# Optimization experiments

Hardware: AMD Instinct MI355X
Metric: run time of the kernel (lower is better)

The kernel has to match this reference:

```python
import jax, jax.numpy as jnp
import numpy as np

N = [80000, 70000, 50000]   # entities per type (flattened over the ragged batch)
F = [64, 128, 48]           # feature width per entity type
D = 512                     # d_model
B = 64                      # number of episodes in the ragged batch
EPS_IN = 1e-4               # InputNorm eps
EPS_LN = 1e-5               # LayerNorm eps
CLIP = 5.0                  # InputNorm cliprange


def setup_inputs() -> dict:
    key = jax.random.key(0)
    ks = jax.random.split(key, 3 * 7 + 2)
    inp = {}
    for i, (n, f) in enumerate(zip(N, F)):
        base = 7 * i
        inp[f"ent{i}"] = jax.random.normal(ks[base], (n, f), dtype=jnp.float32)
        inp[f"mean{i}"] = 0.1 * jax.random.normal(ks[base + 1], (f,), dtype=jnp.float32)
        inp[f"var{i}"] = jax.random.uniform(ks[base + 2], (f,), minval=0.5, maxval=1.5, dtype=jnp.float32)
        inp[f"W{i}"] = jax.random.normal(ks[base + 3], (f, D), dtype=jnp.float32) / np.sqrt(f)
        inp[f"b{i}"] = jnp.zeros((D,), dtype=jnp.float32)
        inp[f"gamma{i}"] = jnp.ones((D,), dtype=jnp.float32)
        inp[f"beta{i}"] = jnp.zeros((D,), dtype=jnp.float32)
    total = sum(N)
    # index_map: permutation reassembling per-type blocks into ragged episode order
    inp["index_map"] = jax.random.permutation(ks[-2], total).astype(jnp.int64)
    inp["batch_index"] = jnp.sort(jax.random.randint(ks[-1], (total,), 0, B)).astype(jnp.int64)
    return inp


def _embed(x, mean, var, W, b, gamma, beta):
    # InputNorm: normalize with running stats, clip outliers
    h = jnp.clip((x - mean) * jax.lax.rsqrt(var + EPS_IN), -CLIP, CLIP)
    # Linear + ReLU
    h = jnp.maximum(h @ W + b, 0.0)
    # LayerNorm
    mu = h.mean(-1, keepdims=True)
    v = ((h - mu) ** 2).mean(-1, keepdims=True)
    return gamma * (h - mu) * jax.lax.rsqrt(v + EPS_LN) + beta


def reference(ent0, mean0, var0, W0, b0, gamma0, beta0,
              ent1, mean1, var1, W1, b1, gamma1, beta1,
              ent2, mean2, var2, W2, b2, gamma2, beta2,
              index_map, batch_index):
    embeds = [
        _embed(ent0, mean0, var0, W0, b0, gamma0, beta0),
        _embed(ent1, mean1, var1, W1, b1, gamma1, beta1),
        _embed(ent2, mean2, var2, W2, b2, gamma2, beta2),
    ]
    x = jnp.concatenate(embeds, axis=0)                      # [sum(N), D]
    entity_type = jnp.concatenate(
        [jnp.full((n, 1), float(i), dtype=jnp.float32) for i, n in enumerate(N)], axis=0
    )
    # ragged reorder: gather-based reassembly into episode-major order
    x = x[index_map]
    entity_types = entity_type[index_map]
    tbatch_index = batch_index[index_map]
    return x, tbatch_index, entity_types
```

## Files before the change

### kernel.cpp

```cpp
#include <hip/hip_runtime.h>

#define DMODEL 512
#define EPS_IN 1e-4f
#define EPS_LN 1e-5f
#define CLIPV  5.0f

typedef float f32x4 __attribute__((ext_vector_type(4)));
typedef short s16x8 __attribute__((ext_vector_type(8)));

__device__ __forceinline__ unsigned short f2bf(float f) {
    union { float f; unsigned u; } v; v.f = f;
    unsigned r = v.u + 0x7fffu + ((v.u >> 16) & 1u);
    return (unsigned short)(r >> 16);
}

struct TypeParams {
    const float* x;
    const float* ss;
    const unsigned short* Wt;
    const float* b; const float* gamma; const float* beta;
    int n;
    int offset;
    int nb;
};

__global__ __launch_bounds__(256) void setup_all(
    const int* __restrict__ index_map, const int* __restrict__ batch_index,
    int* __restrict__ inv, float* __restrict__ out_t, float* __restrict__ out_e,
    int total, int n0, int n01, int nbA,
    const float* __restrict__ W0, const float* __restrict__ W1, const float* __restrict__ W2,
    unsigned short* __restrict__ Wt0, unsigned short* __restrict__ Wt1, unsigned short* __restrict__ Wt2,
    const float* __restrict__ mean0, const float* __restrict__ var0,
    const float* __restrict__ mean1, const float* __restrict__ var1,
    const float* __restrict__ mean2, const float* __restrict__ var2,
    float* __restrict__ ss0, float* __restrict__ ss1, float* __restrict__ ss2)
{
    const int nbB = (DMODEL * 256) / 256;
    if (blockIdx.x < (unsigned)nbA) {
        const int j = blockIdx.x * 256 + threadIdx.x;
        if (j >= total) return;
        const int r = index_map[j];
        inv[r] = j;
        out_t[j] = (float)batch_index[r];
        out_e[j] = (r < n0) ? 0.0f : ((r < n01) ? 1.0f : 2.0f);
    } else if (blockIdx.x < (unsigned)(nbA + nbB)) {
        int idx = (blockIdx.x - nbA) * 256 + threadIdx.x;
        const float* W; unsigned short* Wt; int K, Kp;
        if (idx < DMODEL * 64)              { W = W0; Wt = Wt0; K = 64;  Kp = 64; }
        else if (idx < DMODEL * (64 + 128)) { idx -= DMODEL * 64;  W = W1; Wt = Wt1; K = 128; Kp = 128; }
        else                                { idx -= DMODEL * 192; W = W2; Wt = Wt2; K = 48;  Kp = 64; }
        const int nn = idx / Kp, k = idx - nn * Kp;
        const float w = (k < K) ? W[(size_t)k * DMODEL + nn] : 0.0f;
        Wt[idx] = f2bf(w);
    } else {
        const int c = threadIdx.x;
        if (c < 64)  { const float s = rsqrtf(var0[c] + EPS_IN); ss0[c] = s; ss0[64 + c]  = -mean0[c] * s; }
        if (c < 128) { const float s = rsqrtf(var1[c] + EPS_IN); ss1[c] = s; ss1[128 + c] = -mean1[c] * s; }
        if (c < 48)  { const float s = rsqrtf(var2[c] + EPS_IN); ss2[c] = s; ss2[48 + c]  = -mean2[c] * s; }
    }
}

template<int F, int KP>
__device__ __forceinline__ void embed_body(
    const TypeParams& p, int bid, const int* __restrict__ inv,
    float* __restrict__ out, char* lds)
{
    const int tid  = threadIdx.x;
    const int lane = tid & 63;
    const int wn   = tid >> 6;
    const int l15  = lane & 15;
    const int g    = lane >> 4;
    const int row0 = bid * 32;
    const int n    = p.n;
    constexpr int SEG = KP / 8;
    constexpr int NKS = KP / 32;

    float2* red = reinterpret_cast<float2*>(lds + NKS * 2048);

    if (tid < 32 * SEG) {
        const int r = tid & 31;
        const int s = tid >> 5;
        const int gr = row0 + r;
        const int c = s * 8;
        s16x8 pk;
#pragma unroll
        for (int jj = 0; jj < 8; ++jj) pk[jj] = 0;
        if (gr < n && c < F) {
            const float4 x0 = *(const float4*)(p.x + (size_t)gr * F + c);
            const float4 x1 = *(const float4*)(p.x + (size_t)gr * F + c + 4);
            const float4 sc0 = *(const float4*)(p.ss + c);
            const float4 sc1 = *(const float4*)(p.ss + c + 4);
            const float4 sh0 = *(const float4*)(p.ss + F + c);
            const float4 sh1 = *(const float4*)(p.ss + F + c + 4);
            float t[8];
            t[0] = fmaf(x0.x, sc0.x, sh0.x); t[1] = fmaf(x0.y, sc0.y, sh0.y);
            t[2] = fmaf(x0.z, sc0.z, sh0.z); t[3] = fmaf(x0.w, sc0.w, sh0.w);
            t[4] = fmaf(x1.x, sc1.x, sh1.x); t[5] = fmaf(x1.y, sc1.y, sh1.y);
            t[6] = fmaf(x1.z, sc1.z, sh1.z); t[7] = fmaf(x1.w, sc1.w, sh1.w);
#pragma unroll
            for (int jj = 0; jj < 8; ++jj)
                pk[jj] = (short)f2bf(fminf(fmaxf(t[jj], -CLIPV), CLIPV));
        }
        *reinterpret_cast<s16x8*>(lds + tid * 16) = pk;
    }
    __syncthreads();

    int orow[2];
#pragma unroll
    for (int m = 0; m < 2; ++m) {
        const int rg = row0 + m * 16 + l15;
        orow[m] = (rg < n) ? inv[p.offset + rg] : -1;
    }

    f32x4 acc[2][4];
#pragma unroll
    for (int m = 0; m < 2; ++m)
#pragma unroll
        for (int t = 0; t < 4; ++t) acc[m][t] = (f32x4)0.0f;

    const unsigned short* wtl = p.Wt + (size_t)(wn * 64 + l15) * KP + g * 8;

#pragma unroll
    for (int ks = 0; ks < NKS; ++ks) {
        const int ab = ((ks * 4 + g) * 32 + l15) * 16;
        const s16x8 a0 = *reinterpret_cast<const s16x8*>(lds + ab);
        const s16x8 a1 = *reinterpret_cast<const s16x8*>(lds + ab + 256);
#pragma unroll
        for (int t = 0; t < 4; ++t) {
            const s16x8 wf = *reinterpret_cast<const s16x8*>(wtl + (size_t)t * 16 * KP + ks * 32);
            acc[0][t] = __builtin_amdgcn_mfma_f32_16x16x32_bf16(wf, a0, acc[0][t], 0, 0, 0);
            acc[1][t] = __builtin_amdgcn_mfma_f32_16x16x32_bf16(wf, a1, acc[1][t], 0, 0, 0);
        }
    }

#pragma unroll
    for (int t = 0; t < 4; ++t) {
        const float4 bb = *(const float4*)(p.b + wn * 64 + t * 16 + g * 4);
#pragma unroll
        for (int m = 0; m < 2; ++m) {
            acc[m][t][0] = fmaxf(acc[m][t][0] + bb.x, 0.0f);
            acc[m][t][1] = fmaxf(acc[m][t][1] + bb.y, 0.0f);
            acc[m][t][2] = fmaxf(acc[m][t][2] + bb.z, 0.0f);
            acc[m][t][3] = fmaxf(acc[m][t][3] + bb.w, 0.0f);
        }
    }

    {
        float ps[2] = {0.0f, 0.0f}, pq[2] = {0.0f, 0.0f};
#pragma unroll
        for (int m = 0; m < 2; ++m)
#pragma unroll
            for (int t = 0; t < 4; ++t)
#pragma unroll
                for (int j = 0; j < 4; ++j) {
                    const float v = acc[m][t][j];
                    ps[m] += v;
                    pq[m] = fmaf(v, v, pq[m]);
                }
#pragma unroll
        for (int m = 0; m < 2; ++m) {
            ps[m] += __shfl_xor(ps[m], 16, 64);
            pq[m] += __shfl_xor(pq[m], 16, 64);
            ps[m] += __shfl_xor(ps[m], 32, 64);
            pq[m] += __shfl_xor(pq[m], 32, 64);
        }
        if (g == 0) {
#pragma unroll
            for (int m = 0; m < 2; ++m)
                red[(m * 16 + l15) * 8 + wn] = make_float2(ps[m], pq[m]);
        }
    }
    __syncthreads();

#pragma unroll
    for (int m = 0; m < 2; ++m) {
        const int od = orow[m];
        if (od < 0) continue;
        const int rl = m * 16 + l15;
        float s = 0.0f, q = 0.0f;
#pragma unroll
        for (int wq = 0; wq < 8; ++wq) { const float2 e = red[rl * 8 + wq]; s += e.x; q += e.y; }
        const float mu = s * (1.0f / DMODEL);
        const float vv = fmaxf(q * (1.0f / DMODEL) - mu * mu, 0.0f);
        const float sc = rsqrtf(vv + EPS_LN);
        float* op = out + (size_t)od * DMODEL + wn * 64 + g * 4;
#pragma unroll
        for (int t = 0; t < 4; ++t) {
            const float4 gg = *(const float4*)(p.gamma + wn * 64 + t * 16 + g * 4);
            const float4 ee = *(const float4*)(p.beta  + wn * 64 + t * 16 + g * 4);
            float4 o;
            o.x = fmaf(gg.x * sc, acc[m][t][0] - mu, ee.x);
            o.y = fmaf(gg.y * sc, acc[m][t][1] - mu, ee.y);
            o.z = fmaf(gg.z * sc, acc[m][t][2] - mu, ee.z);
            o.w = fmaf(gg.w * sc, acc[m][t][3] - mu, ee.w);
            *(float4*)(op + t * 16) = o;
        }
    }
}

__global__ __launch_bounds__(512, 6) void embed_all(
    TypeParams p0, TypeParams p1, TypeParams p2,
    const int* __restrict__ inv, float* __restrict__ out)
{
    extern __shared__ char lds[];
    const int bid = blockIdx.x;
    if (bid < p0.nb)                embed_body<64, 64>  (p0, bid, inv, out, lds);
    else if (bid < p0.nb + p1.nb)   embed_body<128, 128>(p1, bid - p0.nb, inv, out, lds);
    else                            embed_body<48, 64>  (p2, bid - p0.nb - p1.nb, inv, out, lds);
}

extern "C" void kernel_launch(void* const* d_in, const int* in_sizes, int n_in,
                              void* d_out, int out_size, void* d_ws, size_t ws_size,
                              hipStream_t stream)
{
    const int F0 = 64, F1 = 128, F2 = 48;
    const int n0 = in_sizes[0]  / F0;
    const int n1 = in_sizes[7]  / F1;
    const int n2 = in_sizes[14] / F2;
    const int total = n0 + n1 + n2;

    float* out   = (float*)d_out;
    float* out_t = out + (size_t)total * DMODEL;
    float* out_e = out_t + total;

    int* inv = (int*)d_ws;
    unsigned short* Wt0 = (unsigned short*)((char*)d_ws + (((size_t)total * 4 + 255) & ~(size_t)255));
    unsigned short* Wt1 = Wt0 + DMODEL * 64;
    unsigned short* Wt2 = Wt1 + DMODEL * 128;
    float* ss0 = (float*)(Wt2 + DMODEL * 64);
    float* ss1 = ss0 + 128;
    float* ss2 = ss1 + 256;

    const int* index_map   = (const int*)d_in[21];
    const int* batch_index = (const int*)d_in[22];

    const int nbA = (total + 255) / 256;
    const int nbB = (DMODEL * 256) / 256;
    setup_all<<<nbA + nbB + 1, 256, 0, stream>>>(
        index_map, batch_index, inv, out_t, out_e, total, n0, n0 + n1, nbA,
        (const float*)d_in[3], (const float*)d_in[10], (const float*)d_in[17],
        Wt0, Wt1, Wt2,
        (const float*)d_in[1],  (const float*)d_in[2],
        (const float*)d_in[8],  (const float*)d_in[9],
        (const float*)d_in[15], (const float*)d_in[16],
        ss0, ss1, ss2);

    TypeParams p0{(const float*)d_in[0],  ss0, Wt0,
                  (const float*)d_in[4],  (const float*)d_in[5],  (const float*)d_in[6],
                  n0, 0,       (n0 + 31) / 32};
    TypeParams p1{(const float*)d_in[7],  ss1, Wt1,
                  (const float*)d_in[11], (const float*)d_in[12], (const float*)d_in[13],
                  n1, n0,      (n1 + 31) / 32};
    TypeParams p2{(const float*)d_in[14], ss2, Wt2,
                  (const float*)d_in[18], (const float*)d_in[19], (const float*)d_in[20],
                  n2, n0 + n1, (n2 + 31) / 32};

    const int nb = p0.nb + p1.nb + p2.nb;
    const int lds_size = 4 * 2048 + 32 * 8 * sizeof(float2);
    embed_all<<<nb, 512, lds_size, stream>>>(p0, p1, p2, inv, out);
}
```

Before: 185.8 us.

## Build per-type compacted output-order lists so embed tiles write near-contiguous rows

Replaces the scattered inverse-permutation write with a per-block prefix-scan compaction. Each type gets a list of (output row, local input row) pairs, ordered by output position, and these are reserved with atomics. The embed kernel now walks tiles of this list, gathering input rows (small) and writing output rows in roughly increasing order instead of random order. This is meant to improve write locality for the large 512-wide output. It adds a zeroing kernel and atomic ordering that is not deterministic across blocks, and it lowers the occupancy hint from 6 to 4.

```diff
diff --git a/kernel.cpp b/kernel.cpp
--- a/kernel.cpp
+++ b/kernel.cpp
@@ -19,32 +19,85 @@
     const float* ss;
     const unsigned short* Wt;
     const float* b; const float* gamma; const float* beta;
-    int n;
-    int offset;
-    int nb;
+    const int2* jl;
 };
 
-__global__ __launch_bounds__(256) void setup_all(
+__global__ void zero_cur(int* cur) { if (threadIdx.x < 4) cur[threadIdx.x] = 0; }
+
+__global__ __launch_bounds__(256) void prep_all(
     const int* __restrict__ index_map, const int* __restrict__ batch_index,
-    int* __restrict__ inv, float* __restrict__ out_t, float* __restrict__ out_e,
-    int total, int n0, int n01, int nbA,
+    float* __restrict__ out_t, float* __restrict__ out_e,
+    int total, int n0, int n01, int nbC,
     const float* __restrict__ W0, const float* __restrict__ W1, const float* __restrict__ W2,
     unsigned short* __restrict__ Wt0, unsigned short* __restrict__ Wt1, unsigned short* __restrict__ Wt2,
     const float* __restrict__ mean0, const float* __restrict__ var0,
     const float* __restrict__ mean1, const float* __restrict__ var1,
     const float* __restrict__ mean2, const float* __restrict__ var2,
-    float* __restrict__ ss0, float* __restrict__ ss1, float* __restrict__ ss2)
+    float* __restrict__ ss0, float* __restrict__ ss1, float* __restrict__ ss2,
+    int2* __restrict__ jl0, int2* __restrict__ jl1, int2* __restrict__ jl2,
+    int* __restrict__ cur)
 {
-    const int nbB = (DMODEL * 256) / 256;
-    if (blockIdx.x < (unsigned)nbA) {
-        const int j = blockIdx.x * 256 + threadIdx.x;
-        if (j >= total) return;
-        const int r = index_map[j];
-        inv[r] = j;
-        out_t[j] = (float)batch_index[r];
-        out_e[j] = (r < n0) ? 0.0f : ((r < n01) ? 1.0f : 2.0f);
-    } else if (blockIdx.x < (unsigned)(nbA + nbB)) {
-        int idx = (blockIdx.x - nbA) * 256 + threadIdx.x;
+    __shared__ int wtot[4][3];
+    __shared__ int wbase[4][3];
+    __shared__ int gbase[3];
+    int b = blockIdx.x;
+    if (b < nbC) {
+        const int tid = threadIdx.x, lane = tid & 63, wid = tid >> 6;
+        const int jb = b * 2048 + tid * 8;
+        int myt[8], myr[8];
+        int c0 = 0, c1 = 0, c2 = 0;
+#pragma unroll
+        for (int i = 0; i < 8; ++i) {
+            const int j = jb + i;
+            myt[i] = -1; myr[i] = 0;
+            if (j < total) {
+                const int r = index_map[j];
+                out_t[j] = (float)batch_index[r];
+                int t, lr;
+                if (r < n0)       { t = 0; lr = r;       c0++; }
+                else if (r < n01) { t = 1; lr = r - n0;  c1++; }
+                else              { t = 2; lr = r - n01; c2++; }
+                myt[i] = t; myr[i] = lr;
+                out_e[j] = (float)t;
+            }
+        }
+        int v0 = c0, v1 = c1, v2 = c2;
+#pragma unroll
+        for (int off = 1; off < 64; off <<= 1) {
+            const int u0 = __shfl_up(v0, off, 64);
+            const int u1 = __shfl_up(v1, off, 64);
+            const int u2 = __shfl_up(v2, off, 64);
+            if (lane >= off) { v0 += u0; v1 += u1; v2 += u2; }
+        }
+        if (lane == 63) { wtot[wid][0] = v0; wtot[wid][1] = v1; wtot[wid][2] = v2; }
+        __syncthreads();
+        if (tid == 0) {
+            int r0 = 0, r1 = 0, r2 = 0;
+            for (int w = 0; w < 4; ++w) {
+                wbase[w][0] = r0; wbase[w][1] = r1; wbase[w][2] = r2;
+                r0 += wtot[w][0]; r1 += wtot[w][1]; r2 += wtot[w][2];
+            }
+            gbase[0] = atomicAdd(&cur[0], r0);
+            gbase[1] = atomicAdd(&cur[1], r1);
+            gbase[2] = atomicAdd(&cur[2], r2);
+        }
+        __syncthreads();
+        int p0 = gbase[0] + wbase[wid][0] + v0 - c0;
+        int p1 = gbase[1] + wbase[wid][1] + v1 - c1;
+        int p2 = gbase[2] + wbase[wid][2] + v2 - c2;
+#pragma unroll
+        for (int i = 0; i < 8; ++i) {
+            const int t = myt[i];
+            const int2 e = make_int2(jb + i, myr[i]);
+            if (t == 0)      jl0[p0++] = e;
+            else if (t == 1) jl1[p1++] = e;
+            else if (t == 2) jl2[p2++] = e;
+        }
+        return;
+    }
+    b -= nbC;
+    if (b < 512) {
+        int idx = b * 256 + threadIdx.x;
         const float* W; unsigned short* Wt; int K, Kp;
         if (idx < DMODEL * 64)              { W = W0; Wt = Wt0; K = 64;  Kp = 64; }
         else if (idx < DMODEL * (64 + 128)) { idx -= DMODEL * 64;  W = W1; Wt = Wt1; K = 128; Kp = 128; }
@@ -52,42 +105,44 @@
         const int nn = idx / Kp, k = idx - nn * Kp;
         const float w = (k < K) ? W[(size_t)k * DMODEL + nn] : 0.0f;
         Wt[idx] = f2bf(w);
-    } else {
-        const int c = threadIdx.x;
-        if (c < 64)  { const float s = rsqrtf(var0[c] + EPS_IN); ss0[c] = s; ss0[64 + c]  = -mean0[c] * s; }
-        if (c < 128) { const float s = rsqrtf(var1[c] + EPS_IN); ss1[c] = s; ss1[128 + c] = -mean1[c] * s; }
-        if (c < 48)  { const float s = rsqrtf(var2[c] + EPS_IN); ss2[c] = s; ss2[48 + c]  = -mean2[c] * s; }
-    }
+        return;
+    }
+    const int c = threadIdx.x;
+    if (c < 64)  { const float s = rsqrtf(var0[c] + EPS_IN); ss0[c] = s; ss0[64 + c]  = -mean0[c] * s; }
+    if (c < 128) { const float s = rsqrtf(var1[c] + EPS_IN); ss1[c] = s; ss1[128 + c] = -mean1[c] * s; }
+    if (c < 48)  { const float s = rsqrtf(var2[c] + EPS_IN); ss2[c] = s; ss2[48 + c]  = -mean2[c] * s; }
 }
 
 template<int F, int KP>
-__device__ __forceinline__ void embed_body(
-    const TypeParams& p, int bid, const int* __restrict__ inv,
-    float* __restrict__ out, char* lds)
+__device__ __forceinline__ void ebody(
+    const TypeParams& p, int tile, int segN, float* __restrict__ out, char* lds)
 {
+    constexpr int SEG = KP / 8;
+    constexpr int NKS = KP / 32;
     const int tid  = threadIdx.x;
     const int lane = tid & 63;
     const int wn   = tid >> 6;
     const int l15  = lane & 15;
     const int g    = lane >> 4;
-    const int row0 = bid * 32;
-    const int n    = p.n;
-    constexpr int SEG = KP / 8;
-    constexpr int NKS = KP / 32;
-
-    float2* red = reinterpret_cast<float2*>(lds + NKS * 2048);
+    const int base = tile * 32;
+
+    float2* red  = reinterpret_cast<float2*>(lds + 8192);
+    int*    ldsj = reinterpret_cast<int*>(lds + 8192 + 2048);
 
     if (tid < 32 * SEG) {
         const int r = tid & 31;
         const int s = tid >> 5;
-        const int gr = row0 + r;
         const int c = s * 8;
+        const int idx = base + r;
+        int2 e = make_int2(-1, 0);
+        if (idx < segN) e = p.jl[idx];
+        if (s == 0) ldsj[r] = e.x;
         s16x8 pk;
 #pragma unroll
         for (int jj = 0; jj < 8; ++jj) pk[jj] = 0;
-        if (gr < n && c < F) {
-            const float4 x0 = *(const float4*)(p.x + (size_t)gr * F + c);
-            const float4 x1 = *(const float4*)(p.x + (size_t)gr * F + c + 4);
+        if (e.x >= 0 && c < F) {
+            const float4 x0 = *(const float4*)(p.x + (size_t)e.y * F + c);
+            const float4 x1 = *(const float4*)(p.x + (size_t)e.y * F + c + 4);
             const float4 sc0 = *(const float4*)(p.ss + c);
             const float4 sc1 = *(const float4*)(p.ss + c + 4);
             const float4 sh0 = *(const float4*)(p.ss + F + c);
@@ -105,13 +160,6 @@
     }
     __syncthreads();
 
-    int orow[2];
-#pragma unroll
-    for (int m = 0; m < 2; ++m) {
-        const int rg = row0 + m * 16 + l15;
-        orow[m] = (rg < n) ? inv[p.offset + rg] : -1;
-    }
-
     f32x4 acc[2][4];
 #pragma unroll
     for (int m = 0; m < 2; ++m)
@@ -174,7 +222,7 @@
 
 #pragma unroll
     for (int m = 0; m < 2; ++m) {
-        const int od = orow[m];
+        const int od = ldsj[m * 16 + l15];
         if (od < 0) continue;
         const int rl = m * 16 + l15;
         float s = 0.0f, q = 0.0f;
@@ -198,15 +246,17 @@
     }
 }
 
-__global__ __launch_bounds__(512, 6) void embed_all(
+__global__ __launch_bounds__(512, 4) void embed_all(
     TypeParams p0, TypeParams p1, TypeParams p2,
-    const int* __restrict__ inv, float* __restrict__ out)
+    const int* __restrict__ cur, float* __restrict__ out)
 {
-    extern __shared__ char lds[];
+    __shared__ char lds[8192 + 2048 + 128];
+    const int c0 = cur[0], c1 = cur[1], c2 = cur[2];
+    const int nt0 = (c0 + 31) >> 5, nt1 = (c1 + 31) >> 5, nt2 = (c2 + 31) >> 5;
     const int bid = blockIdx.x;
-    if (bid < p0.nb)                embed_body<64, 64>  (p0, bid, inv, out, lds);
-    else if (bid < p0.nb + p1.nb)   embed_body<128, 128>(p1, bid - p0.nb, inv, out, lds);
-    else                            embed_body<48, 64>  (p2, bid - p0.nb - p1.nb, inv, out, lds);
+    if (bid < nt0)                  ebody<64, 64>  (p0, bid, c0, out, lds);
+    else if (bid < nt0 + nt1)       ebody<128, 128>(p1, bid - nt0, c1, out, lds);
+    else if (bid < nt0 + nt1 + nt2) ebody<48, 64>  (p2, bid - nt0 - nt1, c2, out, lds);
 }
 
 extern "C" void kernel_launch(void* const* d_in, const int* in_sizes, int n_in,
@@ -223,39 +273,40 @@
     float* out_t = out + (size_t)total * DMODEL;
     float* out_e = out_t + total;
 
-    int* inv = (int*)d_ws;
-    unsigned short* Wt0 = (unsigned short*)((char*)d_ws + (((size_t)total * 4 + 255) & ~(size_t)255));
+    int* cur = (int*)d_ws;
+    unsigned short* Wt0 = (unsigned short*)((char*)d_ws + 256);
     unsigned short* Wt1 = Wt0 + DMODEL * 64;
     unsigned short* Wt2 = Wt1 + DMODEL * 128;
     float* ss0 = (float*)(Wt2 + DMODEL * 64);
     float* ss1 = ss0 + 128;
     float* ss2 = ss1 + 256;
+    size_t joff = (256 + (size_t)DMODEL * 256 * 2 + 4096 + 255) & ~(size_t)255;
+    int2* jl0 = (int2*)((char*)d_ws + joff);
+    int2* jl1 = jl0 + (n0 + 32);
+    int2* jl2 = jl1 + (n1 + 32);
 
     const int* index_map   = (const int*)d_in[21];
     const int* batch_index = (const int*)d_in[22];
 
-    const int nbA = (total + 255) / 256;
-    const int nbB = (DMODEL * 256) / 256;
-    setup_all<<<nbA + nbB + 1, 256, 0, stream>>>(
-        index_map, batch_index, inv, out_t, out_e, total, n0, n0 + n1, nbA,
+    zero_cur<<<1, 64, 0, stream>>>(cur);
+
+    const int nbC = (total + 2047) / 2048;
+    prep_all<<<nbC + 512 + 1, 256, 0, stream>>>(
+        index_map, batch_index, out_t, out_e, total, n0, n0 + n1, nbC,
         (const float*)d_in[3], (const float*)d_in[10], (const float*)d_in[17],
         Wt0, Wt1, Wt2,
         (const float*)d_in[1],  (const float*)d_in[2],
         (const float*)d_in[8],  (const float*)d_in[9],
         (const float*)d_in[15], (const float*)d_in[16],
-        ss0, ss1, ss2);
+        ss0, ss1, ss2, jl0, jl1, jl2, cur);
 
     TypeParams p0{(const float*)d_in[0],  ss0, Wt0,
-                  (const float*)d_in[4],  (const float*)d_in[5],  (const float*)d_in[6],
-                  n0, 0,       (n0 + 31) / 32};
+                  (const float*)d_in[4],  (const float*)d_in[5],  (const float*)d_in[6],  jl0};
     TypeParams p1{(const float*)d_in[7],  ss1, Wt1,
-                  (const float*)d_in[11], (const float*)d_in[12], (const float*)d_in[13],
-                  n1, n0,      (n1 + 31) / 32};
+                  (const float*)d_in[11], (const float*)d_in[12], (const float*)d_in[13], jl1};
     TypeParams p2{(const float*)d_in[14], ss2, Wt2,
-                  (const float*)d_in[18], (const float*)d_in[19], (const float*)d_in[20],
-                  n2, n0 + n1, (n2 + 31) / 32};
-
-    const int nb = p0.nb + p1.nb + p2.nb;
-    const int lds_size = 4 * 2048 + 32 * 8 * sizeof(float2);
-    embed_all<<<nb, 512, lds_size, stream>>>(p0, p1, p2, inv, out);
-}
+                  (const float*)d_in[18], (const float*)d_in[19], (const float*)d_in[20], jl2};
+
+    const int nbE = (total + 31) / 32 + 3;
+    embed_all<<<nbE, 512, 0, stream>>>(p0, p1, p2, cur, out);
+}
```

Measured after the change: 199.0 us. 1.07x slower.
